# Performance work log

Hardware: AMD Instinct MI355X
Metric: run time of the kernel (lower is better)

## Reference

```python
import jax, jax.numpy as jnp
import numpy as np
import math

B, S, H, L, N, V = 4, 2048, 1024, 4, 4, 256
D = H // N
EPS = 1e-5


def setup_inputs() -> dict:
    key = jax.random.key(0)
    ks = iter(jax.random.split(key, 40))
    sc = 1.0 / math.sqrt(H)
    def w(shape, s=None):
        return jax.random.normal(next(ks), shape, dtype=jnp.float32) * (s if s is not None else sc)
    inp = {
        "input_ids": jax.random.randint(next(ks), (B, S), 0, V, dtype=jnp.int32),
        "embed": w((V, H), 0.02),
        "nm_gate_w": w((H, H)), "nm_gate_b": jnp.zeros((H,), jnp.float32),
        "nm_filter_w": w((H, H)), "nm_filter_b": jnp.zeros((H,), jnp.float32),
        "nm_ctx_w": w((2, H)), "nm_ctx_b": jnp.zeros((2,), jnp.float32),
        "q_w": w((L, H, H)), "q_b": jnp.zeros((L, H), jnp.float32),
        "k_w": w((L, H, H)), "k_b": jnp.zeros((L, H), jnp.float32),
        "v_w": w((L, H, H)), "v_b": jnp.zeros((L, H), jnp.float32),
        "gain_w": w((L, N, H)), "gain_b": jnp.zeros((L, N), jnp.float32),
        "attn_ow": w((L, H, H)), "attn_ob": jnp.zeros((L, H), jnp.float32),
        "en_w": w((L, H, H)), "en_b": jnp.zeros((L, H), jnp.float32),
        "plastic_w": w((L, H, H)),
        "fix_w": w((L, H, H)), "fix_b": jnp.zeros((L, H), jnp.float32),
        "ln_g": jnp.ones((L, H), jnp.float32), "ln_b": jnp.zeros((L, H), jnp.float32),
        "out_w": w((V, H)), "out_b": jnp.zeros((V,), jnp.float32),
    }
    return inp


def _forward(input_ids, embed, nm_gate_w, nm_gate_b, nm_filter_w, nm_filter_b,
             nm_ctx_w, nm_ctx_b, q_w, q_b, k_w, k_b, v_w, v_b, gain_w, gain_b,
             attn_ow, attn_ob, en_w, en_b, plastic_w, fix_w, fix_b, ln_g, ln_b,
             out_w, out_b):
    x = embed[input_ids]                                   # [B,S,H]
    # --- NeurotransmitterModule ---
    ctx = x.mean(axis=1)                                   # [B,H]
    nm = ctx @ nm_ctx_w.T + nm_ctx_b                       # [B,2]
    dop, nor = nm[:, :1], nm[:, 1:]                        # [B,1] each
    gate = jax.nn.sigmoid(x @ nm_gate_w.T + nm_gate_b)
    x = x * (1.0 + dop[:, None, :] * gate)
    noise = jnp.tanh(x @ nm_filter_w.T + nm_filter_b)
    x = x + nor[:, None, :] * noise
    inv_sqrt_d = 1.0 / math.sqrt(D)
    for l in range(L):
        # --- GainControlAttention ---
        q = (x @ q_w[l].T + q_b[l]).reshape(B, S, N, D).transpose(0, 2, 1, 3)
        k = (x @ k_w[l].T + k_b[l]).reshape(B, S, N, D).transpose(0, 2, 1, 3)
        v = (x @ v_w[l].T + v_b[l]).reshape(B, S, N, D).transpose(0, 2, 1, 3)
        gain = x.mean(axis=1) @ gain_w[l].T + gain_b[l]    # [B,N]
        q = q * (1.0 + gain[:, :, None, None])
        scores = jnp.einsum('bnsd,bntd->bnst', q, k) * inv_sqrt_d
        attn = jax.nn.softmax(scores, axis=-1)
        ctxv = jnp.einsum('bnst,bntd->bnsd', attn, v)
        a = ctxv.transpose(0, 2, 1, 3).reshape(B, S, H) @ attn_ow[l].T + attn_ob[l]
        x = x + a
        # --- EnergyConstrainedLayer ---
        x = jax.nn.silu(x @ en_w[l].T + en_b[l])
        # --- NeuroplasticityLayer (eval mode) ---
        x = x + (x @ fix_w[l].T + fix_b[l]) + (x @ plastic_w[l].T)
        # --- LayerNorm ---
        mu = x.mean(axis=-1, keepdims=True)
        var = jnp.mean((x - mu) ** 2, axis=-1, keepdims=True)
        x = (x - mu) * jax.lax.rsqrt(var + EPS) * ln_g[l] + ln_b[l]
    return x @ out_w.T + out_b                             # [B,S,V]


def reference(input_ids, embed, nm_gate_w, nm_gate_b, nm_filter_w, nm_filter_b,
              nm_ctx_w, nm_ctx_b, q_w, q_b, k_w, k_b, v_w, v_b, gain_w, gain_b,
              attn_ow, attn_ob, en_w, en_b, plastic_w, fix_w, fix_b, ln_g, ln_b,
              out_w, out_b):
    return _forward(input_ids, embed, nm_gate_w, nm_gate_b, nm_filter_w,
                    nm_filter_b, nm_ctx_w, nm_ctx_b, q_w, q_b, k_w, k_b, v_w,
                    v_b, gain_w, gain_b, attn_ow, attn_ob, en_w, en_b,
                    plastic_w, fix_w, fix_b, ln_g, ln_b, out_w, out_b)
```

## Files before the change

### kernel.cpp

```cpp
#include <hip/hip_runtime.h>

#define B_ 4
#define S_ 2048
#define H_ 1024
#define L_ 4
#define N_ 4
#define D_ 256
#define V_ 256
#define EPSF 1e-5f
#define WH_ ((size_t)H_ * H_)

typedef __attribute__((ext_vector_type(8))) short short8;
typedef __attribute__((ext_vector_type(4))) float f32x4;

__device__ inline float bf2f(unsigned short u) {
    union { unsigned int ui; float f; } c; c.ui = ((unsigned int)u) << 16; return c.f;
}
__device__ inline unsigned short f2bf(float f) {
    union { float f; unsigned int ui; } c; c.f = f;
    unsigned int u = c.ui;
    unsigned int r = (u + 0x7FFFu + ((u >> 16) & 1u)) >> 16;
    return (unsigned short)r;
}
__device__ inline float wave64_sum(float v) {
    for (int m = 32; m >= 1; m >>= 1) v += __shfl_xor(v, m, 64);
    return v;
}
__device__ inline void gl_lds16(const unsigned short* g, unsigned short* l) {
    __builtin_amdgcn_global_load_lds(
        (const __attribute__((address_space(1))) unsigned int*)g,
        (__attribute__((address_space(3))) unsigned int*)l, 16, 0, 0);
}

__global__ void wcvt_kernel(const float* __restrict__ W,
                            unsigned short* __restrict__ Wb, int n8) {
    int idx = blockIdx.x * 256 + threadIdx.x;
    if (idx >= n8) return;
    size_t base = (size_t)idx * 8;
    float4 a0 = *(const float4*)(W + base);
    float4 a1 = *(const float4*)(W + base + 4);
    short8 t;
    t[0] = f2bf(a0.x); t[1] = f2bf(a0.y); t[2] = f2bf(a0.z); t[3] = f2bf(a0.w);
    t[4] = f2bf(a1.x); t[5] = f2bf(a1.y); t[6] = f2bf(a1.z); t[7] = f2bf(a1.w);
    *(short8*)(Wb + base) = t;
}

__global__ void wcvt_qkv(const float* __restrict__ W,
                         unsigned short* __restrict__ Wb, int n8, int sel) {
    int idx = blockIdx.x * 256 + threadIdx.x;
    if (idx >= n8) return;
    size_t p = (size_t)idx * 8;
    size_t layer = p >> 20;
    size_t within = p & (WH_ - 1);
    size_t dst = layer * 3 * WH_ + (size_t)sel * WH_ + within;
    float4 a0 = *(const float4*)(W + p);
    float4 a1 = *(const float4*)(W + p + 4);
    short8 t;
    t[0] = f2bf(a0.x); t[1] = f2bf(a0.y); t[2] = f2bf(a0.z); t[3] = f2bf(a0.w);
    t[4] = f2bf(a1.x); t[5] = f2bf(a1.y); t[6] = f2bf(a1.z); t[7] = f2bf(a1.w);
    *(short8*)(Wb + dst) = t;
}

__global__ void wadd_kernel(const float* __restrict__ Wa, const float* __restrict__ Wb2,
                            unsigned short* __restrict__ Wo, int n8) {
    int idx = blockIdx.x * 256 + threadIdx.x;
    if (idx >= n8) return;
    size_t base = (size_t)idx * 8;
    short8 t;
#pragma unroll
    for (int e = 0; e < 8; e++) {
        size_t p = base + e;
        int pos = (int)(p & (WH_ - 1));
        float v = Wa[p] + Wb2[p] + (((pos >> 10) == (pos & (H_ - 1))) ? 1.f : 0.f);
        t[e] = f2bf(v);
    }
    *(short8*)(Wo + base) = t;
}

__global__ void gather_kernel(const int* __restrict__ ids,
                              const float* __restrict__ embed,
                              unsigned short* __restrict__ x) {
    size_t idx = (size_t)blockIdx.x * 256 + threadIdx.x;
    int bs = (int)(idx >> 10);
    int h  = (int)(idx & 1023);
    x[idx] = f2bf(embed[(size_t)ids[bs] * H_ + h]);
}

__global__ void mean_kernel(const unsigned short* __restrict__ Xin,
                            float* __restrict__ xmean) {
    int idx = blockIdx.x * 256 + threadIdx.x;
    int b = idx >> 10, h = idx & 1023;
    int s0 = blockIdx.y * 128;
    const unsigned short* p = Xin + ((size_t)b * S_ + s0) * H_ + h;
    float s = 0.f;
    for (int i = 0; i < 128; i++) s += bf2f(p[(size_t)i * H_]);
    atomicAdd(&xmean[idx], s);
}

__global__ void nm_kernel(const float* __restrict__ xmean,
                          const float* __restrict__ w,
                          const float* __restrict__ bias,
                          float* __restrict__ dopnor) {
    int wave = threadIdx.x >> 6, lane = threadIdx.x & 63;
    for (int p = wave; p < 2 * B_; p += 4) {
        int b = p >> 1, j = p & 1;
        float s = 0.f;
        for (int h = lane; h < H_; h += 64) s += xmean[b * H_ + h] * w[j * H_ + h];
        s = wave64_sum(s);
        if (lane == 0) dopnor[p] = s / (float)S_ + bias[j];
    }
}

__global__ void gain_kernel(const float* __restrict__ xmean,
                            const float* __restrict__ gw,
                            const float* __restrict__ gb,
                            float* __restrict__ qscale) {
    int wave = threadIdx.x >> 6, lane = threadIdx.x & 63;
    for (int p = wave; p < B_ * N_; p += 4) {
        int b = p >> 2, n = p & 3;
        float s = 0.f;
        for (int h = lane; h < H_; h += 64) s += xmean[b * H_ + h] * gw[n * H_ + h];
        s = wave64_sum(s);
        if (lane == 0) qscale[p] = (1.f + s / (float)S_ + gb[n]) * 0.0625f;
    }
}

__global__ __launch_bounds__(256) void gemm_bt(
    const unsigned short* __restrict__ A, const unsigned short* __restrict__ W,
    const float* __restrict__ bias, void* __restrict__ Cout,
    const unsigned short* __restrict__ X, const float* __restrict__ scal,
    int K, int Nout, int mode) {
    __shared__ unsigned short As[128 * 32];
    __shared__ unsigned short Bs[128 * 32];
    int tid = threadIdx.x;
    int wave = tid >> 6, lane = tid & 63;
    int quad = lane >> 4, l16 = lane & 15;
    int bm = blockIdx.x * 128;
    int bn = blockIdx.y * 128;
    int mw = (wave >> 1) * 64, nw = (wave & 1) * 64;

    const unsigned short* Ag = A + (size_t)(bm + wave * 16 + (lane >> 2)) * K + (lane & 3) * 8;
    const unsigned short* Wg = W + (size_t)(bn + wave * 16 + (lane >> 2)) * K + (lane & 3) * 8;
    unsigned short* ldsA = As + wave * 512;
    unsigned short* ldsB = Bs + wave * 512;
    size_t rowskip = (size_t)64 * K;

    f32x4 acc[4][4];
#pragma unroll
    for (int i = 0; i < 4; i++)
#pragma unroll
        for (int j = 0; j < 4; j++)
#pragma unroll
            for (int r = 0; r < 4; r++) acc[i][j][r] = 0.f;

    for (int kk = 0; kk < K; kk += 32) {
        __syncthreads();
        gl_lds16(Ag + kk, ldsA);
        gl_lds16(Ag + rowskip + kk, ldsA + 2048);
        gl_lds16(Wg + kk, ldsB);
        gl_lds16(Wg + rowskip + kk, ldsB + 2048);
        __syncthreads();

        short8 af[4], bfr[4];
#pragma unroll
        for (int i = 0; i < 4; i++)
            af[i] = *(const short8*)&As[(mw + i * 16 + l16) * 32 + quad * 8];
#pragma unroll
        for (int j = 0; j < 4; j++)
            bfr[j] = *(const short8*)&Bs[(nw + j * 16 + l16) * 32 + quad * 8];
#pragma unroll
        for (int i = 0; i < 4; i++)
#pragma unroll
            for (int j = 0; j < 4; j++)
                acc[i][j] = __builtin_amdgcn_mfma_f32_16x16x32_bf16(af[i], bfr[j], acc[i][j], 0, 0, 0);
    }

    if (mode == 6) {
#pragma unroll
        for (int i = 0; i < 4; i++) {
#pragma unroll
            for (int j = 0; j < 4; j++) {
                int col = bn + nw + j * 16 + l16;
                float bv = bias ? bias[col] : 0.f;
                int n = col >> 8, d = col & 255;
                int row0 = bm + mw + i * 16 + quad * 4;
                int b = row0 >> 11, s0 = row0 & 2047;
                union { unsigned short u[4]; uint2 v; } pk;
#pragma unroll
                for (int r = 0; r < 4; r++) pk.u[r] = f2bf(acc[i][j][r] + bv);
                *(uint2*)((unsigned short*)Cout +
                          ((size_t)(b * N_ + n) * D_ + d) * S_ + s0) = pk.v;
            }
        }
        return;
    }

#pragma unroll
    for (int i = 0; i < 4; i++) {
#pragma unroll
        for (int j = 0; j < 4; j++) {
            int col = bn + nw + j * 16 + l16;
            float bv = bias ? bias[col] : 0.f;
#pragma unroll
            for (int r = 0; r < 4; r++) {
                int row = bm + mw + i * 16 + quad * 4 + r;
                float v = acc[i][j][r] + bv;
                size_t off = (size_t)row * Nout + col;
                if (mode == 5) {
                    ((float*)Cout)[off] = v;
                    continue;
                }
                float outv;
                if (mode == 0) {
                    outv = v;
                } else if (mode == 1) {
                    float sig = 1.f / (1.f + __expf(-v));
                    float dop = scal[(row >> 11) * 2];
                    outv = bf2f(X[off]) * (1.f + dop * sig);
                } else if (mode == 2) {
                    float nor = scal[(row >> 11) * 2 + 1];
                    outv = bf2f(X[off]) + nor * tanhf(v);
                } else if (mode == 3) {
                    outv = v + bf2f(X[off]);
                } else {
                    outv = v * (1.f / (1.f + __expf(-v)));
                }
                ((unsigned short*)Cout)[off] = f2bf(outv);
            }
        }
    }
}

__global__ __launch_bounds__(256) void gemm_qkv(
    const unsigned short* __restrict__ A, const unsigned short* __restrict__ W,
    const float* __restrict__ qb, const float* __restrict__ kb,
    const float* __restrict__ vbb, unsigned short* __restrict__ Qo,
    unsigned short* __restrict__ Ko, unsigned short* __restrict__ Vt) {
    __shared__ unsigned short As[128 * 32];
    __shared__ unsigned short Bs[128 * 32];
    const int K = H_;
    int tid = threadIdx.x;
    int wave = tid >> 6, lane = tid & 63;
    int quad = lane >> 4, l16 = lane & 15;
    int bm = blockIdx.x * 128;
    int bn = blockIdx.y * 128;
    int mw = (wave >> 1) * 64, nw = (wave & 1) * 64;

    const unsigned short* Ag = A + (size_t)(bm + wave * 16 + (lane >> 2)) * K + (lane & 3) * 8;
    const unsigned short* Wg = W + (size_t)(bn + wave * 16 + (lane >> 2)) * K + (lane & 3) * 8;
    unsigned short* ldsA = As + wave * 512;
    unsigned short* ldsB = Bs + wave * 512;
    size_t rowskip = (size_t)64 * K;

    f32x4 acc[4][4];
#pragma unroll
    for (int i = 0; i < 4; i++)
#pragma unroll
        for (int j = 0; j < 4; j++)
#pragma unroll
            for (int r = 0; r < 4; r++) acc[i][j][r] = 0.f;

    for (int kk = 0; kk < K; kk += 32) {
        __syncthreads();
        gl_lds16(Ag + kk, ldsA);
        gl_lds16(Ag + rowskip + kk, ldsA + 2048);
        gl_lds16(Wg + kk, ldsB);
        gl_lds16(Wg + rowskip + kk, ldsB + 2048);
        __syncthreads();

        short8 af[4], bfr[4];
#pragma unroll
        for (int i = 0; i < 4; i++)
            af[i] = *(const short8*)&As[(mw + i * 16 + l16) * 32 + quad * 8];
#pragma unroll
        for (int j = 0; j < 4; j++)
            bfr[j] = *(const short8*)&Bs[(nw + j * 16 + l16) * 32 + quad * 8];
#pragma unroll
        for (int i = 0; i < 4; i++)
#pragma unroll
            for (int j = 0; j < 4; j++)
                acc[i][j] = __builtin_amdgcn_mfma_f32_16x16x32_bf16(af[i], bfr[j], acc[i][j], 0, 0, 0);
    }

    int sel = (bn + nw) >> 10;
    if (sel == 2) {
#pragma unroll
        for (int i = 0; i < 4; i++) {
#pragma unroll
            for (int j = 0; j < 4; j++) {
                int c2 = ((bn + nw) & 1023) + j * 16 + l16;
                float bv = vbb[c2];
                int n = c2 >> 8, d = c2 & 255;
                int row0 = bm + mw + i * 16 + quad * 4;
                int b = row0 >> 11, s0 = row0 & 2047;
                union { unsigned short u[4]; uint2 v; } pk;
#pragma unroll
                for (int r = 0; r < 4; r++) pk.u[r] = f2bf(acc[i][j][r] + bv);
                *(uint2*)(Vt + ((size_t)(b * N_ + n) * D_ + d) * S_ + s0) = pk.v;
            }
        }
    } else {
        unsigned short* Co = (sel == 0) ? Qo : Ko;
        const float* bias = (sel == 0) ? qb : kb;
#pragma unroll
        for (int i = 0; i < 4; i++) {
#pragma unroll
            for (int j = 0; j < 4; j++) {
                int c2 = ((bn + nw) & 1023) + j * 16 + l16;
                float bv = bias[c2];
#pragma unroll
                for (int r = 0; r < 4; r++) {
                    int row = bm + mw + i * 16 + quad * 4 + r;
                    Co[(size_t)row * H_ + c2] = f2bf(acc[i][j][r] + bv);
                }
            }
        }
    }
}

__global__ __launch_bounds__(256) void flash_attn(
    const unsigned short* __restrict__ Q, const unsigned short* __restrict__ Kg,
    const unsigned short* __restrict__ VT, const float* __restrict__ qscale,
    unsigned short* __restrict__ O) {
    __shared__ unsigned short Kt[64][264];
    __shared__ unsigned short Vtl[272][72];
    __shared__ unsigned short Pl[4][32][72];

    int tid = threadIdx.x;
    int wave = tid >> 6, lane = tid & 63;
    int quad = lane >> 4, l16 = lane & 15;
    int bnh = blockIdx.y;
    size_t base = ((size_t)(bnh >> 2) * S_) * H_ + (size_t)(bnh & 3) * D_;
    size_t vtbase = (size_t)bnh * D_ * S_;
    int qw = blockIdx.x * 128 + wave * 32;
    float scale = qscale[bnh];

    for (int c = tid; c < 16 * 72; c += 256) {
        int rr = c / 72, cc = c - rr * 72;
        Vtl[256 + rr][cc] = (rr == 0) ? (unsigned short)0x3F80 : (unsigned short)0;
    }

    short8 qf[2][8];
#pragma unroll
    for (int rt = 0; rt < 2; rt++)
#pragma unroll
        for (int kk = 0; kk < 8; kk++)
            qf[rt][kk] = *(const short8*)(Q + base +
                (size_t)(qw + rt * 16 + l16) * H_ + kk * 32 + quad * 8);

    f32x4 o[2][16], osum[2];
#pragma unroll
    for (int rt = 0; rt < 2; rt++) {
#pragma unroll
        for (int c = 0; c < 16; c++)
#pragma unroll
            for (int r = 0; r < 4; r++) o[rt][c][r] = 0.f;
#pragma unroll
        for (int r = 0; r < 4; r++) osum[rt][r] = 0.f;
    }
    float mrow[2][4];
#pragma unroll
    for (int rt = 0; rt < 2; rt++)
#pragma unroll
        for (int r = 0; r < 4; r++) mrow[rt][r] = -1e30f;

    for (int t0 = 0; t0 < S_; t0 += 64) {
        __syncthreads();
#pragma unroll
        for (int rr = 0; rr < 8; rr++) {
            int c = rr * 256 + tid;
            int row = c >> 5, col = (c & 31) * 8;
            *(short8*)&Kt[row][col] =
                *(const short8*)(Kg + base + (size_t)(t0 + row) * H_ + col);
        }
#pragma unroll
        for (int rr = 0; rr < 8; rr++) {
            int c = rr * 256 + tid;
            int d = c >> 3, col = (c & 7) * 8;
            *(short8*)&Vtl[d][col] =
                *(const short8*)(VT + vtbase + (size_t)d * S_ + t0 + col);
        }
        __syncthreads();

        f32x4 s0[4], s1[4];
#pragma unroll
        for (int j = 0; j < 4; j++)
#pragma unroll
            for (int r = 0; r < 4; r++) { s0[j][r] = 0.f; s1[j][r] = 0.f; }
#pragma unroll
        for (int j = 0; j < 4; j++)
#pragma unroll
            for (int kk = 0; kk < 8; kk++) {
                short8 kf = *(const short8*)&Kt[j * 16 + l16][kk * 32 + quad * 8];
                s0[j] = __builtin_amdgcn_mfma_f32_16x16x32_bf16(qf[0][kk], kf, s0[j], 0, 0, 0);
                s1[j] = __builtin_amdgcn_mfma_f32_16x16x32_bf16(qf[1][kk], kf, s1[j], 0, 0, 0);
            }

#pragma unroll
        for (int rt = 0; rt < 2; rt++) {
            float alpha[4];
#pragma unroll
            for (int r = 0; r < 4; r++) {
                float sv[4];
#pragma unroll
                for (int j = 0; j < 4; j++)
                    sv[j] = (rt == 0 ? s0[j][r] : s1[j][r]) * scale;
                float mx = fmaxf(fmaxf(sv[0], sv[1]), fmaxf(sv[2], sv[3]));
                for (int m = 8; m >= 1; m >>= 1) mx = fmaxf(mx, __shfl_xor(mx, m, 64));
                float mnew = fmaxf(mrow[rt][r], mx);
                alpha[r] = __expf(mrow[rt][r] - mnew);
                mrow[rt][r] = mnew;
#pragma unroll
                for (int j = 0; j < 4; j++)
                    Pl[wave][rt * 16 + quad * 4 + r][j * 16 + l16] =
                        f2bf(__expf(sv[j] - mnew));
            }
#pragma unroll
            for (int c = 0; c < 16; c++)
#pragma unroll
                for (int r = 0; r < 4; r++) o[rt][c][r] *= alpha[r];
#pragma unroll
            for (int r = 0; r < 4; r++) osum[rt][r] *= alpha[r];
        }

        short8 pf[2][2];
#pragma unroll
        for (int rt = 0; rt < 2; rt++) {
            pf[rt][0] = *(const short8*)&Pl[wave][rt * 16 + l16][quad * 8];
            pf[rt][1] = *(const short8*)&Pl[wave][rt * 16 + l16][32 + quad * 8];
        }
#pragma unroll
        for (int c = 0; c < 16; c++) {
            short8 vf0 = *(const short8*)&Vtl[c * 16 + l16][quad * 8];
            o[0][c] = __builtin_amdgcn_mfma_f32_16x16x32_bf16(pf[0][0], vf0, o[0][c], 0, 0, 0);
            o[1][c] = __builtin_amdgcn_mfma_f32_16x16x32_bf16(pf[1][0], vf0, o[1][c], 0, 0, 0);
            short8 vf1 = *(const short8*)&Vtl[c * 16 + l16][32 + quad * 8];
            o[0][c] = __builtin_amdgcn_mfma_f32_16x16x32_bf16(pf[0][1], vf1, o[0][c], 0, 0, 0);
            o[1][c] = __builtin_amdgcn_mfma_f32_16x16x32_bf16(pf[1][1], vf1, o[1][c], 0, 0, 0);
        }
        {
            short8 vs0 = *(const short8*)&Vtl[256 + l16][quad * 8];
            short8 vs1 = *(const short8*)&Vtl[256 + l16][32 + quad * 8];
            osum[0] = __builtin_amdgcn_mfma_f32_16x16x32_bf16(pf[0][0], vs0, osum[0], 0, 0, 0);
            osum[0] = __builtin_amdgcn_mfma_f32_16x16x32_bf16(pf[0][1], vs1, osum[0], 0, 0, 0);
            osum[1] = __builtin_amdgcn_mfma_f32_16x16x32_bf16(pf[1][0], vs0, osum[1], 0, 0, 0);
            osum[1] = __builtin_amdgcn_mfma_f32_16x16x32_bf16(pf[1][1], vs1, osum[1], 0, 0, 0);
        }
    }

#pragma unroll
    for (int rt = 0; rt < 2; rt++) {
        float invl[4];
#pragma unroll
        for (int r = 0; r < 4; r++)
            invl[r] = 1.f / __shfl(osum[rt][r], (lane & 48), 64);
#pragma unroll
        for (int c = 0; c < 16; c++)
#pragma unroll
            for (int r = 0; r < 4; r++) {
                int row = qw + rt * 16 + quad * 4 + r;
                int d = c * 16 + l16;
                O[base + (size_t)row * H_ + d] = f2bf(o[rt][c][r] * invl[r]);
            }
    }
}

__global__ __launch_bounds__(256) void ln_kernel(
    const unsigned short* __restrict__ y, const float* __restrict__ g,
    const float* __restrict__ bta, unsigned short* __restrict__ out) {
    int row = blockIdx.x;
    size_t ro = (size_t)row * H_;
    int tid = threadIdx.x;
    float t[4]; float s = 0.f, s2 = 0.f;
#pragma unroll
    for (int i = 0; i < 4; i++) {
        int h = i * 256 + tid;
        float v = bf2f(y[ro + h]);
        t[i] = v; s += v; s2 += v * v;
    }
    s = wave64_sum(s); s2 = wave64_sum(s2);
    __shared__ float sh[8];
    int wave = tid >> 6, lane = tid & 63;
    if (lane == 0) { sh[wave] = s; sh[4 + wave] = s2; }
    __syncthreads();
    s  = sh[0] + sh[1] + sh[2] + sh[3];
    s2 = sh[4] + sh[5] + sh[6] + sh[7];
    float mu = s * (1.f / H_);
    float var = s2 * (1.f / H_) - mu * mu;
    float inv = rsqrtf(var + EPSF);
#pragma unroll
    for (int i = 0; i < 4; i++) {
        int h = i * 256 + tid;
        out[ro + h] = f2bf((t[i] - mu) * inv * g[h] + bta[h]);
    }
}

extern "C" void kernel_launch(void* const* d_in, const int* in_sizes, int n_in,
                              void* d_out, int out_size, void* d_ws, size_t ws_size,
                              hipStream_t stream) {
    const int*   ids          = (const int*)d_in[0];
    const float* embed        = (const float*)d_in[1];
    const float* nm_gate_w    = (const float*)d_in[2];
    const float* nm_gate_b    = (const float*)d_in[3];
    const float* nm_filter_w  = (const float*)d_in[4];
    const float* nm_filter_b  = (const float*)d_in[5];
    const float* nm_ctx_w     = (const float*)d_in[6];
    const float* nm_ctx_b     = (const float*)d_in[7];
    const float* q_w          = (const float*)d_in[8];
    const float* q_b          = (const float*)d_in[9];
    const float* k_w          = (const float*)d_in[10];
    const float* k_b          = (const float*)d_in[11];
    const float* v_w          = (const float*)d_in[12];
    const float* v_b          = (const float*)d_in[13];
    const float* gain_w       = (const float*)d_in[14];
    const float* gain_b       = (const float*)d_in[15];
    const float* attn_ow      = (const float*)d_in[16];
    const float* attn_ob      = (const float*)d_in[17];
    const float* en_w         = (const float*)d_in[18];
    const float* en_b         = (const float*)d_in[19];
    const float* plastic_w    = (const float*)d_in[20];
    const float* fix_w        = (const float*)d_in[21];
    const float* fix_b        = (const float*)d_in[22];
    const float* ln_g         = (const float*)d_in[23];
    const float* ln_b         = (const float*)d_in[24];
    const float* out_w        = (const float*)d_in[25];
    const float* out_b        = (const float*)d_in[26];

    size_t T  = (size_t)B_ * S_ * H_;
    size_t smallBytes = ((size_t)B_ * H_ + 2 * B_ + B_ * N_ + 8) * sizeof(float);
    size_t megaElems  = 26 * WH_ + WH_ / 4;
    size_t need_base  = 4 * T * 2 + smallBytes + 2 * WH_;
    size_t need_mega  = 4 * T * 2 + smallBytes + 2 * megaElems;
    if (ws_size < need_base) return;
    bool mega = ws_size >= need_mega;

    unsigned short* X   = (unsigned short*)d_ws;
    unsigned short* Qb  = X + T;
    unsigned short* Kb  = Qb + T;
    unsigned short* Vb  = Kb + T;
    float* xmean  = (float*)(Vb + T);
    float* dopnor = xmean + (size_t)B_ * H_;
    float* qscale = dopnor + 2 * B_;
    unsigned short* Wbase = (unsigned short*)(qscale + B_ * N_ + 8);
#define WOFF(k) (Wbase + (size_t)(k) * WH_)

    const int M   = B_ * S_;
    const int W8  = (int)(WH_ / 8);
    const int WG  = (W8 + 255) / 256;
    const int W84 = (int)(4 * WH_ / 8);
    const int WG4 = (W84 + 255) / 256;
    const int W8o = V_ * H_ / 8;
    const int WGo = (W8o + 255) / 256;

    if (mega) {
        wcvt_kernel<<<WG,  256, 0, stream>>>(nm_gate_w,   WOFF(0), W8);
        wcvt_kernel<<<WG,  256, 0, stream>>>(nm_filter_w, WOFF(1), W8);
        wcvt_qkv<<<WG4, 256, 0, stream>>>(q_w, WOFF(2), W84, 0);
        wcvt_qkv<<<WG4, 256, 0, stream>>>(k_w, WOFF(2), W84, 1);
        wcvt_qkv<<<WG4, 256, 0, stream>>>(v_w, WOFF(2), W84, 2);
        wcvt_kernel<<<WG4, 256, 0, stream>>>(attn_ow, WOFF(14), W84);
        wcvt_kernel<<<WG4, 256, 0, stream>>>(en_w,    WOFF(18), W84);
        wadd_kernel<<<WG4, 256, 0, stream>>>(fix_w, plastic_w, WOFF(22), W84);
        wcvt_kernel<<<WGo, 256, 0, stream>>>(out_w, WOFF(26), W8o);
    }

    gather_kernel<<<dim3((int)(T / 256)), 256, 0, stream>>>(ids, embed, X);

    hipMemsetAsync(xmean, 0, (size_t)B_ * H_ * sizeof(float), stream);
    mean_kernel<<<dim3(B_ * H_ / 256, 16), 256, 0, stream>>>(X, xmean);
    nm_kernel<<<1, 256, 0, stream>>>(xmean, nm_ctx_w, nm_ctx_b, dopnor);

    const unsigned short* Wp;
    if (mega) Wp = WOFF(0);
    else { wcvt_kernel<<<WG, 256, 0, stream>>>(nm_gate_w, Wbase, W8); Wp = Wbase; }
    gemm_bt<<<dim3(M / 128, H_ / 128), 256, 0, stream>>>(
        X, Wp, nm_gate_b, Qb, X, dopnor, H_, H_, 1);
    if (mega) Wp = WOFF(1);
    else { wcvt_kernel<<<WG, 256, 0, stream>>>(nm_filter_w, Wbase, W8); Wp = Wbase; }
    gemm_bt<<<dim3(M / 128, H_ / 128), 256, 0, stream>>>(
        Qb, Wp, nm_filter_b, X, Qb, dopnor, H_, H_, 2);

    for (int l = 0; l < L_; l++) {
        size_t wo = (size_t)l * WH_;
        size_t bo = (size_t)l * H_;
        hipMemsetAsync(xmean, 0, (size_t)B_ * H_ * sizeof(float), stream);
        mean_kernel<<<dim3(B_ * H_ / 256, 16), 256, 0, stream>>>(X, xmean);
        gain_kernel<<<1, 256, 0, stream>>>(xmean, gain_w + (size_t)l * N_ * H_,
                                           gain_b + (size_t)l * N_, qscale);

        if (mega) {
            gemm_qkv<<<dim3(M / 128, 3 * H_ / 128), 256, 0, stream>>>(
                X, WOFF(2) + (size_t)l * 3 * WH_, q_b + bo, k_b + bo, v_b + bo,
                Qb, Kb, Vb);
        } else {
            wcvt_kernel<<<WG, 256, 0, stream>>>(q_w + wo, Wbase, W8);
            gemm_bt<<<dim3(M / 128, H_ / 128), 256, 0, stream>>>(
                X, Wbase, q_b + bo, Qb, nullptr, nullptr, H_, H_, 0);
            wcvt_kernel<<<WG, 256, 0, stream>>>(k_w + wo, Wbase, W8);
            gemm_bt<<<dim3(M / 128, H_ / 128), 256, 0, stream>>>(
                X, Wbase, k_b + bo, Kb, nullptr, nullptr, H_, H_, 0);
            wcvt_kernel<<<WG, 256, 0, stream>>>(v_w + wo, Wbase, W8);
            gemm_bt<<<dim3(M / 128, H_ / 128), 256, 0, stream>>>(
                X, Wbase, v_b + bo, Vb, nullptr, nullptr, H_, H_, 6);
        }

        flash_attn<<<dim3(S_ / 128, B_ * N_), 256, 0, stream>>>(
            Qb, Kb, Vb, qscale, Qb);

        if (mega) Wp = WOFF(14) + wo;
        else { wcvt_kernel<<<WG, 256, 0, stream>>>(attn_ow + wo, Wbase, W8); Wp = Wbase; }
        gemm_bt<<<dim3(M / 128, H_ / 128), 256, 0, stream>>>(
            Qb, Wp, attn_ob + bo, Kb, X, nullptr, H_, H_, 3);
        if (mega) Wp = WOFF(18) + wo;
        else { wcvt_kernel<<<WG, 256, 0, stream>>>(en_w + wo, Wbase, W8); Wp = Wbase; }
        gemm_bt<<<dim3(M / 128, H_ / 128), 256, 0, stream>>>(
            Kb, Wp, en_b + bo, Vb, nullptr, nullptr, H_, H_, 4);
        if (mega) Wp = WOFF(22) + wo;
        else { wadd_kernel<<<WG, 256, 0, stream>>>(fix_w + wo, plastic_w + wo, Wbase, W8); Wp = Wbase; }
        gemm_bt<<<dim3(M / 128, H_ / 128), 256, 0, stream>>>(
            Vb, Wp, fix_b + bo, Qb, nullptr, nullptr, H_, H_, 0);
        ln_kernel<<<dim3(M), 256, 0, stream>>>(Qb, ln_g + bo, ln_b + bo, X);
    }

    if (mega) Wp = WOFF(26);
    else { wcvt_kernel<<<WGo, 256, 0, stream>>>(out_w, Wbase, W8o); Wp = Wbase; }
    gemm_bt<<<dim3(M / 128, V_ / 128), 256, 0, stream>>>(
        X, Wp, out_b, (float*)d_out, nullptr, nullptr, H_, V_, 5);
#undef WOFF
}
```

Measured before the change: 1.924 ms.

## Use 8 waves of 16 query rows in flash attention with lazy rescaling

The flash attention kernel now runs 512 threads per block, with each of 8 waves owning 16 query rows instead of 4 waves owning 32. This halves per-wave accumulator registers and doubles the waves sharing each K/V tile in LDS, aiming for more latency hiding with the same grid. It also skips the online-softmax rescale of the output accumulators when the new tile maximum stays within 8 of the running maximum, a wave-uniform branch that saves multiplies. In exchange each wave's K/V fragment reads feed half as many MFMAs, and skipped rescaling risks larger exponent values in bf16 P.

```diff
diff --git a/kernel.cpp b/kernel.cpp
--- a/kernel.cpp
+++ b/kernel.cpp
@@ -318,13 +318,13 @@
     }
 }
 
-__global__ __launch_bounds__(256) void flash_attn(
+__global__ __launch_bounds__(512) void flash_attn(
     const unsigned short* __restrict__ Q, const unsigned short* __restrict__ Kg,
     const unsigned short* __restrict__ VT, const float* __restrict__ qscale,
     unsigned short* __restrict__ O) {
     __shared__ unsigned short Kt[64][264];
     __shared__ unsigned short Vtl[272][72];
-    __shared__ unsigned short Pl[4][32][72];
+    __shared__ unsigned short Pl[8][16][72];
 
     int tid = threadIdx.x;
     int wave = tid >> 6, lane = tid & 63;
@@ -332,137 +332,129 @@
     int bnh = blockIdx.y;
     size_t base = ((size_t)(bnh >> 2) * S_) * H_ + (size_t)(bnh & 3) * D_;
     size_t vtbase = (size_t)bnh * D_ * S_;
-    int qw = blockIdx.x * 128 + wave * 32;
+    int qw = blockIdx.x * 128 + wave * 16;
     float scale = qscale[bnh];
 
-    for (int c = tid; c < 16 * 72; c += 256) {
+    for (int c = tid; c < 16 * 72; c += 512) {
         int rr = c / 72, cc = c - rr * 72;
         Vtl[256 + rr][cc] = (rr == 0) ? (unsigned short)0x3F80 : (unsigned short)0;
     }
 
-    short8 qf[2][8];
-#pragma unroll
-    for (int rt = 0; rt < 2; rt++)
-#pragma unroll
-        for (int kk = 0; kk < 8; kk++)
-            qf[rt][kk] = *(const short8*)(Q + base +
-                (size_t)(qw + rt * 16 + l16) * H_ + kk * 32 + quad * 8);
-
-    f32x4 o[2][16], osum[2];
-#pragma unroll
-    for (int rt = 0; rt < 2; rt++) {
-#pragma unroll
-        for (int c = 0; c < 16; c++)
-#pragma unroll
-            for (int r = 0; r < 4; r++) o[rt][c][r] = 0.f;
-#pragma unroll
-        for (int r = 0; r < 4; r++) osum[rt][r] = 0.f;
-    }
-    float mrow[2][4];
-#pragma unroll
-    for (int rt = 0; rt < 2; rt++)
-#pragma unroll
-        for (int r = 0; r < 4; r++) mrow[rt][r] = -1e30f;
+    short8 qf[8];
+#pragma unroll
+    for (int kk = 0; kk < 8; kk++)
+        qf[kk] = *(const short8*)(Q + base +
+            (size_t)(qw + l16) * H_ + kk * 32 + quad * 8);
+
+    f32x4 o[16], osum;
+#pragma unroll
+    for (int c = 0; c < 16; c++)
+#pragma unroll
+        for (int r = 0; r < 4; r++) o[c][r] = 0.f;
+#pragma unroll
+    for (int r = 0; r < 4; r++) osum[r] = 0.f;
+    float mrow[4];
+#pragma unroll
+    for (int r = 0; r < 4; r++) mrow[r] = -1e30f;
 
     for (int t0 = 0; t0 < S_; t0 += 64) {
         __syncthreads();
 #pragma unroll
-        for (int rr = 0; rr < 8; rr++) {
-            int c = rr * 256 + tid;
+        for (int rr = 0; rr < 4; rr++) {
+            int c = rr * 512 + tid;
             int row = c >> 5, col = (c & 31) * 8;
             *(short8*)&Kt[row][col] =
                 *(const short8*)(Kg + base + (size_t)(t0 + row) * H_ + col);
         }
 #pragma unroll
-        for (int rr = 0; rr < 8; rr++) {
-            int c = rr * 256 + tid;
+        for (int rr = 0; rr < 4; rr++) {
+            int c = rr * 512 + tid;
             int d = c >> 3, col = (c & 7) * 8;
             *(short8*)&Vtl[d][col] =
                 *(const short8*)(VT + vtbase + (size_t)d * S_ + t0 + col);
         }
         __syncthreads();
 
-        f32x4 s0[4], s1[4];
+        f32x4 s[4];
 #pragma unroll
         for (int j = 0; j < 4; j++)
 #pragma unroll
-            for (int r = 0; r < 4; r++) { s0[j][r] = 0.f; s1[j][r] = 0.f; }
+            for (int r = 0; r < 4; r++) s[j][r] = 0.f;
 #pragma unroll
         for (int j = 0; j < 4; j++)
 #pragma unroll
             for (int kk = 0; kk < 8; kk++) {
                 short8 kf = *(const short8*)&Kt[j * 16 + l16][kk * 32 + quad * 8];
-                s0[j] = __builtin_amdgcn_mfma_f32_16x16x32_bf16(qf[0][kk], kf, s0[j], 0, 0, 0);
-                s1[j] = __builtin_amdgcn_mfma_f32_16x16x32_bf16(qf[1][kk], kf, s1[j], 0, 0, 0);
+                s[j] = __builtin_amdgcn_mfma_f32_16x16x32_bf16(qf[kk], kf, s[j], 0, 0, 0);
             }
 
-#pragma unroll
-        for (int rt = 0; rt < 2; rt++) {
+        float sv[4][4], mx[4];
+        bool ok = true;
+#pragma unroll
+        for (int r = 0; r < 4; r++) {
+#pragma unroll
+            for (int j = 0; j < 4; j++) sv[r][j] = s[j][r] * scale;
+            float m0 = fmaxf(fmaxf(sv[r][0], sv[r][1]), fmaxf(sv[r][2], sv[r][3]));
+            for (int m = 8; m >= 1; m >>= 1) m0 = fmaxf(m0, __shfl_xor(m0, m, 64));
+            mx[r] = m0;
+            ok = ok && (m0 <= mrow[r] + 8.f);
+        }
+        if (__all(ok)) {
+#pragma unroll
+            for (int r = 0; r < 4; r++)
+#pragma unroll
+                for (int j = 0; j < 4; j++)
+                    Pl[wave][quad * 4 + r][j * 16 + l16] =
+                        f2bf(__expf(sv[r][j] - mrow[r]));
+        } else {
             float alpha[4];
 #pragma unroll
             for (int r = 0; r < 4; r++) {
-                float sv[4];
+                float mnew = fmaxf(mrow[r], mx[r]);
+                alpha[r] = __expf(mrow[r] - mnew);
+                mrow[r] = mnew;
 #pragma unroll
                 for (int j = 0; j < 4; j++)
-                    sv[j] = (rt == 0 ? s0[j][r] : s1[j][r]) * scale;
-                float mx = fmaxf(fmaxf(sv[0], sv[1]), fmaxf(sv[2], sv[3]));
-                for (int m = 8; m >= 1; m >>= 1) mx = fmaxf(mx, __shfl_xor(mx, m, 64));
-                float mnew = fmaxf(mrow[rt][r], mx);
-                alpha[r] = __expf(mrow[rt][r] - mnew);
-                mrow[rt][r] = mnew;
-#pragma unroll
-                for (int j = 0; j < 4; j++)
-                    Pl[wave][rt * 16 + quad * 4 + r][j * 16 + l16] =
-                        f2bf(__expf(sv[j] - mnew));
+                    Pl[wave][quad * 4 + r][j * 16 + l16] =
+                        f2bf(__expf(sv[r][j] - mnew));
             }
 #pragma unroll
             for (int c = 0; c < 16; c++)
 #pragma unroll
-                for (int r = 0; r < 4; r++) o[rt][c][r] *= alpha[r];
-#pragma unroll
-            for (int r = 0; r < 4; r++) osum[rt][r] *= alpha[r];
-        }
-
-        short8 pf[2][2];
-#pragma unroll
-        for (int rt = 0; rt < 2; rt++) {
-            pf[rt][0] = *(const short8*)&Pl[wave][rt * 16 + l16][quad * 8];
-            pf[rt][1] = *(const short8*)&Pl[wave][rt * 16 + l16][32 + quad * 8];
-        }
+                for (int r = 0; r < 4; r++) o[c][r] *= alpha[r];
+#pragma unroll
+            for (int r = 0; r < 4; r++) osum[r] *= alpha[r];
+        }
+
+        short8 pf0 = *(const short8*)&Pl[wave][l16][quad * 8];
+        short8 pf1 = *(const short8*)&Pl[wave][l16][32 + quad * 8];
 #pragma unroll
         for (int c = 0; c < 16; c++) {
             short8 vf0 = *(const short8*)&Vtl[c * 16 + l16][quad * 8];
-            o[0][c] = __builtin_amdgcn_mfma_f32_16x16x32_bf16(pf[0][0], vf0, o[0][c], 0, 0, 0);
-            o[1][c] = __builtin_amdgcn_mfma_f32_16x16x32_bf16(pf[1][0], vf0, o[1][c], 0, 0, 0);
+            o[c] = __builtin_amdgcn_mfma_f32_16x16x32_bf16(pf0, vf0, o[c], 0, 0, 0);
             short8 vf1 = *(const short8*)&Vtl[c * 16 + l16][32 + quad * 8];
-            o[0][c] = __builtin_amdgcn_mfma_f32_16x16x32_bf16(pf[0][1], vf1, o[0][c], 0, 0, 0);
-            o[1][c] = __builtin_amdgcn_mfma_f32_16x16x32_bf16(pf[1][1], vf1, o[1][c], 0, 0, 0);
+            o[c] = __builtin_amdgcn_mfma_f32_16x16x32_bf16(pf1, vf1, o[c], 0, 0, 0);
         }
         {
             short8 vs0 = *(const short8*)&Vtl[256 + l16][quad * 8];
             short8 vs1 = *(const short8*)&Vtl[256 + l16][32 + quad * 8];
-            osum[0] = __builtin_amdgcn_mfma_f32_16x16x32_bf16(pf[0][0], vs0, osum[0], 0, 0, 0);
-            osum[0] = __builtin_amdgcn_mfma_f32_16x16x32_bf16(pf[0][1], vs1, osum[0], 0, 0, 0);
-            osum[1] = __builtin_amdgcn_mfma_f32_16x16x32_bf16(pf[1][0], vs0, osum[1], 0, 0, 0);
-            osum[1] = __builtin_amdgcn_mfma_f32_16x16x32_bf16(pf[1][1], vs1, osum[1], 0, 0, 0);
-        }
-    }
-
-#pragma unroll
-    for (int rt = 0; rt < 2; rt++) {
-        float invl[4];
-#pragma unroll
-        for (int r = 0; r < 4; r++)
-            invl[r] = 1.f / __shfl(osum[rt][r], (lane & 48), 64);
-#pragma unroll
-        for (int c = 0; c < 16; c++)
-#pragma unroll
-            for (int r = 0; r < 4; r++) {
-                int row = qw + rt * 16 + quad * 4 + r;
-                int d = c * 16 + l16;
-                O[base + (size_t)row * H_ + d] = f2bf(o[rt][c][r] * invl[r]);
-            }
-    }
+            osum = __builtin_amdgcn_mfma_f32_16x16x32_bf16(pf0, vs0, osum, 0, 0, 0);
+            osum = __builtin_amdgcn_mfma_f32_16x16x32_bf16(pf1, vs1, osum, 0, 0, 0);
+        }
+    }
+
+    float invl[4];
+#pragma unroll
+    for (int r = 0; r < 4; r++)
+        invl[r] = 1.f / __shfl(osum[r], (lane & 48), 64);
+#pragma unroll
+    for (int c = 0; c < 16; c++)
+#pragma unroll
+        for (int r = 0; r < 4; r++) {
+            int row = qw + quad * 4 + r;
+            int d = c * 16 + l16;
+            O[base + (size_t)row * H_ + d] = f2bf(o[c][r] * invl[r]);
+        }
 }
 
 __global__ __launch_bounds__(256) void ln_kernel(
@@ -604,7 +596,7 @@
                 X, Wbase, v_b + bo, Vb, nullptr, nullptr, H_, H_, 6);
         }
 
-        flash_attn<<<dim3(S_ / 128, B_ * N_), 256, 0, stream>>>(
+        flash_attn<<<dim3(S_ / 128, B_ * N_), 512, 0, stream>>>(
             Qb, Kb, Vb, qscale, Qb);
 
         if (mega) Wp = WOFF(14) + wo;
```

After: 1.789 ms. 7.0% less time.
